# Kernel tuning notes

Measured on AMD Instinct MI355X. Metric: run time of the kernel, lower is better.

## Reference

```python
import jax, jax.numpy as jnp
import numpy as np

FP8_MAX = 448.0  # e4m3 max (use_e4m3=True)
FP8_DTYPE = jnp.float8_e4m3fn


def _quant_dequant(t):
    # scale = fp8_max / clamp(amax, 1e-12); quantize with clamp + fp8 cast; dequantize with 1/scale
    amax = jnp.maximum(jnp.abs(t).max(), 1e-12)
    scale = FP8_MAX / amax
    q = jnp.clip(t * scale, -FP8_MAX, FP8_MAX).astype(FP8_DTYPE)
    return q.astype(jnp.float32) * (1.0 / scale)


def setup_inputs() -> dict:
    key = jax.random.key(0)
    k1, k2 = jax.random.split(key)
    x = jax.random.normal(k1, (8, 2048, 4096), dtype=jnp.float32)
    weight = jax.random.normal(k2, (4096, 4096), dtype=jnp.float32) * 0.02  # (K, N)
    return {"x": x, "weight": weight}


def reference(x, weight):
    bsz, seqlen, K = x.shape
    x2d = x.reshape(-1, K)                    # (M, K)
    a32 = _quant_dequant(x2d)                 # fp8 round-trip of activations
    w32_t = _quant_dequant(weight.T)          # fp8 round-trip of transposed weight (N, K)
    out = a32 @ w32_t.T                       # (M, N) fp32 GEMM
    return out.astype(x.dtype).reshape(bsz, seqlen, -1)
```

## Files before the change

### kernel.cpp

```cpp
#include <hip/hip_runtime.h>
#include <hip/hip_bf16.h>

#define M_DIM 16384
#define N_DIM 4096
#define K_DIM 4096
#define FP8_MAX 448.0f

#define BM 256
#define BN 256
#define NK64 (K_DIM / 64)

typedef float f32x16 __attribute__((ext_vector_type(16)));
typedef int i32x4 __attribute__((ext_vector_type(4)));
typedef int i32x8 __attribute__((ext_vector_type(8)));


__global__ void init_amax_kernel(unsigned* amax) {
    if (threadIdx.x < 2) amax[threadIdx.x] = 0u;
}

__global__ void amax2_kernel(const float* __restrict__ x,
                             const float* __restrict__ w,
                             unsigned* __restrict__ amax) {
    const float* p;
    long n4;
    unsigned* out;
    long bid, nb;
    if (blockIdx.x < 2048) {
        p = x; n4 = (long)M_DIM * K_DIM / 4; out = amax + 0;
        bid = blockIdx.x; nb = 2048;
    } else {
        p = w; n4 = (long)K_DIM * N_DIM / 4; out = amax + 1;
        bid = blockIdx.x - 2048; nb = 1024;
    }
    float m = 0.f;
    const float4* p4 = (const float4*)p;
    for (long i = bid * blockDim.x + threadIdx.x; i < n4; i += nb * blockDim.x) {
        float4 v = p4[i];
        m = fmaxf(m, fmaxf(fmaxf(fabsf(v.x), fabsf(v.y)),
                           fmaxf(fabsf(v.z), fabsf(v.w))));
    }
#pragma unroll
    for (int off = 32; off > 0; off >>= 1)
        m = fmaxf(m, __shfl_down(m, off));
    __shared__ float smax[4];
    int lane = threadIdx.x & 63, wid = threadIdx.x >> 6;
    if (lane == 0) smax[wid] = m;
    __syncthreads();
    if (threadIdx.x == 0) {
        float bm = fmaxf(fmaxf(smax[0], smax[1]), fmaxf(smax[2], smax[3]));
        atomicMax(out, __float_as_uint(bm));
    }
}

__device__ __forceinline__ unsigned pack4(float4 v, float s) {
    float a = fminf(fmaxf(v.x * s, -FP8_MAX), FP8_MAX);
    float b = fminf(fmaxf(v.y * s, -FP8_MAX), FP8_MAX);
    float c = fminf(fmaxf(v.z * s, -FP8_MAX), FP8_MAX);
    float d = fminf(fmaxf(v.w * s, -FP8_MAX), FP8_MAX);
    int p = 0;
    p = __builtin_amdgcn_cvt_pk_fp8_f32(a, b, p, false);
    p = __builtin_amdgcn_cvt_pk_fp8_f32(c, d, p, true);
    return (unsigned)p;
}

__global__ void quant_kernel(const float* __restrict__ x,
                             const float* __restrict__ w,
                             unsigned char* __restrict__ qa,
                             unsigned char* __restrict__ qw,
                             const unsigned* __restrict__ amax) {
    __shared__ unsigned tile[64][17];
    int t = threadIdx.x;
    if (blockIdx.x < 512) {
        float scale = FP8_MAX / fmaxf(__uint_as_float(amax[0]), 1e-12f);
        int m32 = blockIdx.x;
        int lane = t & 63;
        int g = t >> 6;
        int m = m32 * 32 + (lane & 31);
        int kh = lane >> 5;
        const float* rp = x + (long)m * K_DIM;
        unsigned char* ob = qa + (long)m32 * NK64 * 2048;
#pragma unroll
        for (int it = 0; it < 16; ++it) {
            int k64 = it * 4 + g;
            int kb = k64 * 64 + kh * 32;
            float4 v0 = *(const float4*)&rp[kb];
            float4 v1 = *(const float4*)&rp[kb + 4];
            float4 v2 = *(const float4*)&rp[kb + 8];
            float4 v3 = *(const float4*)&rp[kb + 12];
            float4 v4 = *(const float4*)&rp[kb + 16];
            float4 v5 = *(const float4*)&rp[kb + 20];
            float4 v6 = *(const float4*)&rp[kb + 24];
            float4 v7 = *(const float4*)&rp[kb + 28];
            uint4 o0, o1;
            o0.x = pack4(v0, scale); o0.y = pack4(v1, scale);
            o0.z = pack4(v2, scale); o0.w = pack4(v3, scale);
            o1.x = pack4(v4, scale); o1.y = pack4(v5, scale);
            o1.z = pack4(v6, scale); o1.w = pack4(v7, scale);
            *(uint4*)&ob[(long)k64 * 2048 + lane * 16] = o0;
            *(uint4*)&ob[(long)k64 * 2048 + 1024 + lane * 16] = o1;
        }
    } else {
        float scale = FP8_MAX / fmaxf(__uint_as_float(amax[1]), 1e-12f);
        int b = blockIdx.x - 512;
        int bk = b & 63, bn = b >> 6;
        int k0 = bk * 64, n0 = bn * 64;
#pragma unroll
        for (int pass = 0; pass < 4; ++pass) {
            int idx = pass * 256 + t;
            int k = idx >> 4, nw = idx & 15;
            float4 v = *(const float4*)&w[(long)(k0 + k) * N_DIM + n0 + nw * 4];
            tile[k][nw] = pack4(v, scale);
        }
        __syncthreads();
        int lane = t & 63, g = t >> 6;
        int n32 = g >> 1, h = g & 1;
        int nl = n32 * 32 + (lane & 31);
        int word = nl >> 2, sh = (nl & 3) * 8;
        int kb = (lane >> 5) * 32 + h * 16;
        uint4 o;
        unsigned* ow = (unsigned*)&o;
#pragma unroll
        for (int wd = 0; wd < 4; ++wd) {
            unsigned acc = 0;
#pragma unroll
            for (int j = 0; j < 4; ++j)
                acc |= ((tile[kb + wd * 4 + j][word] >> sh) & 0xffu) << (8 * j);
            ow[wd] = acc;
        }
        long gn32 = (long)(n0 >> 5) + n32;
        *(uint4*)&qw[(gn32 * NK64 + bk) * 2048 + h * 1024 + lane * 16] = o;
    }
}

__device__ __forceinline__ void stage_q(const unsigned char* __restrict__ Aseg,
                                        const unsigned char* __restrict__ Bseg,
                                        unsigned char* stbuf, int tid, int kt, int r) {
    int c = r * 512 + tid;
    int f = (c >> 7) & 7;
    int q = c & 127;
    const unsigned char* src =
        ((c < 1024) ? Aseg : Bseg) + ((long)f * NK64 + kt) * 2048 + q * 16;
    __builtin_amdgcn_global_load_lds(
        (const __attribute__((address_space(1))) void*)src,
        (__attribute__((address_space(3))) void*)(stbuf + c * 16), 16, 0, 0);
}

__device__ __forceinline__ i32x8 comb(i32x4 lo, i32x4 hi) {
    return __builtin_shufflevector(lo, hi, 0, 1, 2, 3, 4, 5, 6, 7);
}

template <int VW, bool STG, bool NEXT>
__device__ __forceinline__ void tile_step(
    unsigned char* sbase, const unsigned char* __restrict__ Aseg,
    const unsigned char* __restrict__ Bseg, int kt, int tid, int lane,
    int wm, int wn, i32x4 (&ca)[4][2], i32x4 (&cb)[2][2],
    i32x4 (&na)[4][2], i32x4 (&nb)[2][2], f32x16 (&acc)[4][2]) {
    if constexpr (VW == 4)
        asm volatile("s_waitcnt vmcnt(4) lgkmcnt(0)" ::: "memory");
    else if constexpr (VW == 0)
        asm volatile("s_waitcnt vmcnt(0) lgkmcnt(0)" ::: "memory");
    if constexpr (VW >= 0) {
        __builtin_amdgcn_sched_barrier(0);
        __builtin_amdgcn_s_barrier();
        __builtin_amdgcn_sched_barrier(0);
    }

    if constexpr (NEXT) {
        const unsigned char* nbuf = sbase + (size_t)((kt + 1) & 3) * 32768;
        const unsigned char* nAl = nbuf + wm * 4 * 2048;
        const unsigned char* nBl = nbuf + 16384 + wn * 2 * 2048;
#pragma unroll
        for (int i = 0; i < 4; ++i) {
            na[i][0] = *(const i32x4*)(nAl + i * 2048 + lane * 16);
            na[i][1] = *(const i32x4*)(nAl + i * 2048 + 1024 + lane * 16);
        }
#pragma unroll
        for (int j = 0; j < 2; ++j) {
            nb[j][0] = *(const i32x4*)(nBl + j * 2048 + lane * 16);
            nb[j][1] = *(const i32x4*)(nBl + j * 2048 + 1024 + lane * 16);
        }
    }
    if constexpr (STG) {
        unsigned char* stbuf = sbase + (size_t)((kt + 3) & 3) * 32768;
        stage_q(Aseg, Bseg, stbuf, tid, kt + 3, 0);
        stage_q(Aseg, Bseg, stbuf, tid, kt + 3, 1);
        stage_q(Aseg, Bseg, stbuf, tid, kt + 3, 2);
        stage_q(Aseg, Bseg, stbuf, tid, kt + 3, 3);
    }
    __builtin_amdgcn_sched_barrier(0);
    __builtin_amdgcn_s_setprio(1);
#pragma unroll
    for (int i = 0; i < 4; ++i)
        acc[i][0] = __builtin_amdgcn_mfma_scale_f32_32x32x64_f8f6f4(
            comb(ca[i][0], ca[i][1]), comb(cb[0][0], cb[0][1]), acc[i][0],
            0, 0, 0, 0x7f7f7f7f, 0, 0x7f7f7f7f);
#pragma unroll
    for (int i = 0; i < 4; ++i)
        acc[i][1] = __builtin_amdgcn_mfma_scale_f32_32x32x64_f8f6f4(
            comb(ca[i][0], ca[i][1]), comb(cb[1][0], cb[1][1]), acc[i][1],
            0, 0, 0, 0x7f7f7f7f, 0, 0x7f7f7f7f);
    __builtin_amdgcn_s_setprio(0);
}

__global__ __launch_bounds__(512, 2) void gemm_fp8_kernel(
    const unsigned char* __restrict__ qa, const unsigned char* __restrict__ qw,
    float* __restrict__ out, const unsigned* __restrict__ amax) {
    __shared__ unsigned char lds[4][32768];

    int b = blockIdx.x;
    int swz = (b & 7) * 128 + (b >> 3);
    int bm = swz >> 4;
    int bn = swz & 15;

    int tid = threadIdx.x;
    int lane = tid & 63;
    int w = tid >> 6;
    int wm = w >> 2, wn = w & 3;

    f32x16 acc[4][2];
#pragma unroll
    for (int i = 0; i < 4; ++i)
#pragma unroll
        for (int j = 0; j < 2; ++j) acc[i][j] = (f32x16)0.f;

    const unsigned char* Aseg = qa + (long)(bm * 8) * NK64 * 2048;
    const unsigned char* Bseg = qw + (long)(bn * 8) * NK64 * 2048;
    unsigned char* sbase = &lds[0][0];

    i32x4 A0[4][2], B0[2][2], A1[4][2], B1[2][2];

#pragma unroll
    for (int pt = 0; pt < 3; ++pt)
#pragma unroll
        for (int r = 0; r < 4; ++r)
            stage_q(Aseg, Bseg, sbase + (size_t)pt * 32768, tid, pt, r);
    asm volatile("s_waitcnt vmcnt(0)" ::: "memory");
    __builtin_amdgcn_sched_barrier(0);
    __builtin_amdgcn_s_barrier();
    __builtin_amdgcn_sched_barrier(0);
    {
        const unsigned char* Al = sbase + wm * 4 * 2048 + lane * 16;
        const unsigned char* Bl = sbase + 16384 + wn * 2 * 2048 + lane * 16;
#pragma unroll
        for (int i = 0; i < 4; ++i) {
            A0[i][0] = *(const i32x4*)(Al + i * 2048);
            A0[i][1] = *(const i32x4*)(Al + i * 2048 + 1024);
        }
#pragma unroll
        for (int j = 0; j < 2; ++j) {
            B0[j][0] = *(const i32x4*)(Bl + j * 2048);
            B0[j][1] = *(const i32x4*)(Bl + j * 2048 + 1024);
        }
    }

    tile_step<-1, true, true>(sbase, Aseg, Bseg, 0, tid, lane, wm, wn,
                              A0, B0, A1, B1, acc);
#pragma unroll 1
    for (int kt = 1; kt < 61; kt += 2) {
        tile_step<4, true, true>(sbase, Aseg, Bseg, kt, tid, lane, wm, wn,
                                 A1, B1, A0, B0, acc);
        tile_step<4, true, true>(sbase, Aseg, Bseg, kt + 1, tid, lane, wm, wn,
                                 A0, B0, A1, B1, acc);
    }
    tile_step<4, false, true>(sbase, Aseg, Bseg, 61, tid, lane, wm, wn,
                              A1, B1, A0, B0, acc);
    tile_step<0, false, true>(sbase, Aseg, Bseg, 62, tid, lane, wm, wn,
                              A0, B0, A1, B1, acc);
    tile_step<-1, false, false>(sbase, Aseg, Bseg, 63, tid, lane, wm, wn,
                                A1, B1, A0, B0, acc);

    float ax = fmaxf(__uint_as_float(amax[0]), 1e-12f);
    float aw = fmaxf(__uint_as_float(amax[1]), 1e-12f);
    float s = ax * aw * (1.0f / (FP8_MAX * FP8_MAX));

    long m0 = (long)bm * BM + wm * 128;
    long n0 = (long)bn * BN + wn * 64;
    int col = lane & 31;
    int rbase = 4 * (lane >> 5);
#pragma unroll
    for (int i = 0; i < 4; ++i)
#pragma unroll
        for (int j = 0; j < 2; ++j)
#pragma unroll
            for (int reg = 0; reg < 16; ++reg) {
                int row = (reg & 3) + 8 * (reg >> 2) + rbase;
                out[(m0 + i * 32 + row) * N_DIM + n0 + j * 32 + col] =
                    acc[i][j][reg] * s;
            }
}

extern "C" void kernel_launch(void* const* d_in, const int* in_sizes, int n_in,
                              void* d_out, int out_size, void* d_ws, size_t ws_size,
                              hipStream_t stream) {
    const float* x = (const float*)d_in[0];
    const float* wgt = (const float*)d_in[1];
    float* out = (float*)d_out;

    unsigned* amax = (unsigned*)d_ws;
    unsigned char* qa = (unsigned char*)d_ws + 256;
    unsigned char* qw = qa + (long)M_DIM * K_DIM;

    init_amax_kernel<<<1, 64, 0, stream>>>(amax);
    amax2_kernel<<<3072, 256, 0, stream>>>(x, wgt, amax);
    quant_kernel<<<4608, 256, 0, stream>>>(x, wgt, qa, qw, amax);

    dim3 grid((M_DIM / BM) * (N_DIM / BN));
    gemm_fp8_kernel<<<grid, 512, 0, stream>>>(qa, qw, out, amax);
}
```

Before: 444.5 us.

## Halve GEMM block tile to 128x256 with triple-buffered LDS and higher occupancy

Shrinks the FP8 GEMM block tile from 256x256 to 128x256. Each wave now holds a 2x2 grid of MFMA accumulators instead of 4x2. The 4-deep LDS ring of 32KB buffers becomes a 3-deep ring of 24KB buffers, and the register-level double buffering of fragments is removed: fragments are loaded from LDS right before use. Launch bounds are raised to target 4 blocks per CU to hide latency through occupancy. The trade-off is lower data reuse per block, more global traffic, and fewer MFMAs between barriers.

```diff
diff --git a/kernel.cpp b/kernel.cpp
--- a/kernel.cpp
+++ b/kernel.cpp
@@ -6,9 +6,10 @@
 #define K_DIM 4096
 #define FP8_MAX 448.0f
 
-#define BM 256
+#define BM 128
 #define BN 256
 #define NK64 (K_DIM / 64)
+#define BUFB 24576
 
 typedef float f32x16 __attribute__((ext_vector_type(16)));
 typedef int i32x4 __attribute__((ext_vector_type(4)));
@@ -135,81 +136,78 @@
 
 __device__ __forceinline__ void stage_q(const unsigned char* __restrict__ Aseg,
                                         const unsigned char* __restrict__ Bseg,
-                                        unsigned char* stbuf, int tid, int kt, int r) {
-    int c = r * 512 + tid;
-    int f = (c >> 7) & 7;
-    int q = c & 127;
-    const unsigned char* src =
-        ((c < 1024) ? Aseg : Bseg) + ((long)f * NK64 + kt) * 2048 + q * 16;
-    __builtin_amdgcn_global_load_lds(
-        (const __attribute__((address_space(1))) void*)src,
-        (__attribute__((address_space(3))) void*)(stbuf + c * 16), 16, 0, 0);
+                                        unsigned char* stbuf, int tid, int kt) {
+#pragma unroll
+    for (int r = 0; r < 3; ++r) {
+        int c = r * 512 + tid;
+        const unsigned char* src;
+        if (c < 512)
+            src = Aseg + ((long)(c >> 7) * NK64 + kt) * 2048 + (c & 127) * 16;
+        else
+            src = Bseg + ((long)((c - 512) >> 7) * NK64 + kt) * 2048 + (c & 127) * 16;
+        __builtin_amdgcn_global_load_lds(
+            (const __attribute__((address_space(1))) void*)src,
+            (__attribute__((address_space(3))) void*)(stbuf + c * 16), 16, 0, 0);
+    }
 }
 
 __device__ __forceinline__ i32x8 comb(i32x4 lo, i32x4 hi) {
     return __builtin_shufflevector(lo, hi, 0, 1, 2, 3, 4, 5, 6, 7);
 }
 
-template <int VW, bool STG, bool NEXT>
+#define SB() __builtin_amdgcn_sched_barrier(0)
+
+template <int VW, bool STG>
 __device__ __forceinline__ void tile_step(
     unsigned char* sbase, const unsigned char* __restrict__ Aseg,
     const unsigned char* __restrict__ Bseg, int kt, int tid, int lane,
-    int wm, int wn, i32x4 (&ca)[4][2], i32x4 (&cb)[2][2],
-    i32x4 (&na)[4][2], i32x4 (&nb)[2][2], f32x16 (&acc)[4][2]) {
-    if constexpr (VW == 4)
-        asm volatile("s_waitcnt vmcnt(4) lgkmcnt(0)" ::: "memory");
-    else if constexpr (VW == 0)
+    int wm, int wn, f32x16 (&acc)[2][2]) {
+    if constexpr (VW == 3)
+        asm volatile("s_waitcnt vmcnt(3) lgkmcnt(0)" ::: "memory");
+    else
         asm volatile("s_waitcnt vmcnt(0) lgkmcnt(0)" ::: "memory");
-    if constexpr (VW >= 0) {
-        __builtin_amdgcn_sched_barrier(0);
-        __builtin_amdgcn_s_barrier();
-        __builtin_amdgcn_sched_barrier(0);
-    }
-
-    if constexpr (NEXT) {
-        const unsigned char* nbuf = sbase + (size_t)((kt + 1) & 3) * 32768;
-        const unsigned char* nAl = nbuf + wm * 4 * 2048;
-        const unsigned char* nBl = nbuf + 16384 + wn * 2 * 2048;
-#pragma unroll
-        for (int i = 0; i < 4; ++i) {
-            na[i][0] = *(const i32x4*)(nAl + i * 2048 + lane * 16);
-            na[i][1] = *(const i32x4*)(nAl + i * 2048 + 1024 + lane * 16);
-        }
-#pragma unroll
-        for (int j = 0; j < 2; ++j) {
-            nb[j][0] = *(const i32x4*)(nBl + j * 2048 + lane * 16);
-            nb[j][1] = *(const i32x4*)(nBl + j * 2048 + 1024 + lane * 16);
-        }
-    }
-    if constexpr (STG) {
-        unsigned char* stbuf = sbase + (size_t)((kt + 3) & 3) * 32768;
-        stage_q(Aseg, Bseg, stbuf, tid, kt + 3, 0);
-        stage_q(Aseg, Bseg, stbuf, tid, kt + 3, 1);
-        stage_q(Aseg, Bseg, stbuf, tid, kt + 3, 2);
-        stage_q(Aseg, Bseg, stbuf, tid, kt + 3, 3);
-    }
-    __builtin_amdgcn_sched_barrier(0);
+    SB();
+    __builtin_amdgcn_s_barrier();
+    SB();
+
+    const unsigned char* buf = sbase + (size_t)(kt % 3) * BUFB;
+    const unsigned char* Al = buf + (wm * 2) * 2048 + lane * 16;
+    const unsigned char* Bl = buf + 8192 + (wn * 2) * 2048 + lane * 16;
+
+    i32x4 a[2][2], bb[2][2];
+#pragma unroll
+    for (int i = 0; i < 2; ++i) {
+        a[i][0] = *(const i32x4*)(Al + i * 2048);
+        a[i][1] = *(const i32x4*)(Al + i * 2048 + 1024);
+    }
+#pragma unroll
+    for (int j = 0; j < 2; ++j) {
+        bb[j][0] = *(const i32x4*)(Bl + j * 2048);
+        bb[j][1] = *(const i32x4*)(Bl + j * 2048 + 1024);
+    }
+    if constexpr (STG)
+        stage_q(Aseg, Bseg, sbase + (size_t)((kt + 2) % 3) * BUFB, tid, kt + 2);
+    SB();
+    asm volatile("s_waitcnt lgkmcnt(0)" ::: "memory");
+    SB();
     __builtin_amdgcn_s_setprio(1);
 #pragma unroll
-    for (int i = 0; i < 4; ++i)
-        acc[i][0] = __builtin_amdgcn_mfma_scale_f32_32x32x64_f8f6f4(
-            comb(ca[i][0], ca[i][1]), comb(cb[0][0], cb[0][1]), acc[i][0],
-            0, 0, 0, 0x7f7f7f7f, 0, 0x7f7f7f7f);
-#pragma unroll
-    for (int i = 0; i < 4; ++i)
-        acc[i][1] = __builtin_amdgcn_mfma_scale_f32_32x32x64_f8f6f4(
-            comb(ca[i][0], ca[i][1]), comb(cb[1][0], cb[1][1]), acc[i][1],
-            0, 0, 0, 0x7f7f7f7f, 0, 0x7f7f7f7f);
+    for (int i = 0; i < 2; ++i)
+#pragma unroll
+        for (int j = 0; j < 2; ++j)
+            acc[i][j] = __builtin_amdgcn_mfma_scale_f32_32x32x64_f8f6f4(
+                comb(a[i][0], a[i][1]), comb(bb[j][0], bb[j][1]), acc[i][j],
+                0, 0, 0, 0x7f7f7f7f, 0, 0x7f7f7f7f);
     __builtin_amdgcn_s_setprio(0);
 }
 
-__global__ __launch_bounds__(512, 2) void gemm_fp8_kernel(
+__global__ __launch_bounds__(512, 4) void gemm_fp8_kernel(
     const unsigned char* __restrict__ qa, const unsigned char* __restrict__ qw,
     float* __restrict__ out, const unsigned* __restrict__ amax) {
-    __shared__ unsigned char lds[4][32768];
+    __shared__ unsigned char lds[3][BUFB];
 
     int b = blockIdx.x;
-    int swz = (b & 7) * 128 + (b >> 3);
+    int swz = (b & 7) * 256 + (b >> 3);
     int bm = swz >> 4;
     int bn = swz & 15;
 
@@ -218,68 +216,35 @@
     int w = tid >> 6;
     int wm = w >> 2, wn = w & 3;
 
-    f32x16 acc[4][2];
-#pragma unroll
-    for (int i = 0; i < 4; ++i)
+    f32x16 acc[2][2];
+#pragma unroll
+    for (int i = 0; i < 2; ++i)
 #pragma unroll
         for (int j = 0; j < 2; ++j) acc[i][j] = (f32x16)0.f;
 
-    const unsigned char* Aseg = qa + (long)(bm * 8) * NK64 * 2048;
+    const unsigned char* Aseg = qa + (long)(bm * 4) * NK64 * 2048;
     const unsigned char* Bseg = qw + (long)(bn * 8) * NK64 * 2048;
     unsigned char* sbase = &lds[0][0];
 
-    i32x4 A0[4][2], B0[2][2], A1[4][2], B1[2][2];
-
-#pragma unroll
-    for (int pt = 0; pt < 3; ++pt)
-#pragma unroll
-        for (int r = 0; r < 4; ++r)
-            stage_q(Aseg, Bseg, sbase + (size_t)pt * 32768, tid, pt, r);
-    asm volatile("s_waitcnt vmcnt(0)" ::: "memory");
-    __builtin_amdgcn_sched_barrier(0);
-    __builtin_amdgcn_s_barrier();
-    __builtin_amdgcn_sched_barrier(0);
-    {
-        const unsigned char* Al = sbase + wm * 4 * 2048 + lane * 16;
-        const unsigned char* Bl = sbase + 16384 + wn * 2 * 2048 + lane * 16;
-#pragma unroll
-        for (int i = 0; i < 4; ++i) {
-            A0[i][0] = *(const i32x4*)(Al + i * 2048);
-            A0[i][1] = *(const i32x4*)(Al + i * 2048 + 1024);
-        }
-#pragma unroll
-        for (int j = 0; j < 2; ++j) {
-            B0[j][0] = *(const i32x4*)(Bl + j * 2048);
-            B0[j][1] = *(const i32x4*)(Bl + j * 2048 + 1024);
-        }
-    }
-
-    tile_step<-1, true, true>(sbase, Aseg, Bseg, 0, tid, lane, wm, wn,
-                              A0, B0, A1, B1, acc);
+    stage_q(Aseg, Bseg, sbase + 0 * BUFB, tid, 0);
+    stage_q(Aseg, Bseg, sbase + 1 * BUFB, tid, 1);
+
 #pragma unroll 1
-    for (int kt = 1; kt < 61; kt += 2) {
-        tile_step<4, true, true>(sbase, Aseg, Bseg, kt, tid, lane, wm, wn,
-                                 A1, B1, A0, B0, acc);
-        tile_step<4, true, true>(sbase, Aseg, Bseg, kt + 1, tid, lane, wm, wn,
-                                 A0, B0, A1, B1, acc);
-    }
-    tile_step<4, false, true>(sbase, Aseg, Bseg, 61, tid, lane, wm, wn,
-                              A1, B1, A0, B0, acc);
-    tile_step<0, false, true>(sbase, Aseg, Bseg, 62, tid, lane, wm, wn,
-                              A0, B0, A1, B1, acc);
-    tile_step<-1, false, false>(sbase, Aseg, Bseg, 63, tid, lane, wm, wn,
-                                A1, B1, A0, B0, acc);
+    for (int kt = 0; kt < 62; ++kt)
+        tile_step<3, true>(sbase, Aseg, Bseg, kt, tid, lane, wm, wn, acc);
+    tile_step<3, false>(sbase, Aseg, Bseg, 62, tid, lane, wm, wn, acc);
+    tile_step<0, false>(sbase, Aseg, Bseg, 63, tid, lane, wm, wn, acc);
 
     float ax = fmaxf(__uint_as_float(amax[0]), 1e-12f);
     float aw = fmaxf(__uint_as_float(amax[1]), 1e-12f);
     float s = ax * aw * (1.0f / (FP8_MAX * FP8_MAX));
 
-    long m0 = (long)bm * BM + wm * 128;
+    long m0 = (long)bm * BM + wm * 64;
     long n0 = (long)bn * BN + wn * 64;
     int col = lane & 31;
     int rbase = 4 * (lane >> 5);
 #pragma unroll
-    for (int i = 0; i < 4; ++i)
+    for (int i = 0; i < 2; ++i)
 #pragma unroll
         for (int j = 0; j < 2; ++j)
 #pragma unroll
```

After: 457.7 us. +3.0%, slower.
